# Optimization experiments

Hardware: AMD Instinct MI355X
Metric: run time of the kernel (lower is better)

The kernel has to match this reference:

```python
import jax, jax.numpy as jnp
import numpy as np

C_S, C_Z, C_H, H, PQ, PV = 384, 128, 16, 12, 4, 8
B, N = 1, 512
W_C = (2.0 / (9.0 * PQ)) ** 0.5
W_L = (1.0 / 3.0) ** 0.5
OUT_IN = H * C_Z + H * C_H + H * PV * 3 + H * PV  # 2112


def setup_inputs() -> dict:
    key = jax.random.key(0)
    ks = jax.random.split(key, 16)
    s_i = jax.random.normal(ks[0], (B, N, C_S), jnp.float32)
    z_ij = jax.random.normal(ks[1], (B, N, N, C_Z), jnp.float32)
    # random rotation matrices via QR
    raw = jax.random.normal(ks[2], (B, N, 3, 3), jnp.float32)
    q, r = jnp.linalg.qr(raw)
    rots = q * jnp.sign(jnp.diagonal(r, axis1=-2, axis2=-1))[..., None, :]
    trans = jax.random.normal(ks[3], (B, N, 3), jnp.float32)
    sc = lambda fan_in: 1.0 / np.sqrt(fan_in)
    Wq = jax.random.normal(ks[4], (C_S, H * C_H), jnp.float32) * sc(C_S)
    Wk = jax.random.normal(ks[5], (C_S, H * C_H), jnp.float32) * sc(C_S)
    Wv = jax.random.normal(ks[6], (C_S, H * C_H), jnp.float32) * sc(C_S)
    Wqp = jax.random.normal(ks[7], (C_S, H * PQ * 3), jnp.float32) * sc(C_S)
    Wkp = jax.random.normal(ks[8], (C_S, H * PQ * 3), jnp.float32) * sc(C_S)
    Wvp = jax.random.normal(ks[9], (C_S, H * PV * 3), jnp.float32) * sc(C_S)
    Wb = jax.random.normal(ks[10], (C_Z, H), jnp.float32) * sc(C_Z)
    gamma = jax.random.normal(ks[11], (1, 1, 1, H), jnp.float32)
    Wout = jax.random.normal(ks[12], (OUT_IN, C_S), jnp.float32) * sc(OUT_IN)
    bout = jnp.zeros((C_S,), jnp.float32)
    return dict(s_i=s_i, z_ij=z_ij, rots=rots, trans=trans, Wq=Wq, Wk=Wk, Wv=Wv,
                Wqp=Wqp, Wkp=Wkp, Wvp=Wvp, Wb=Wb, gamma=gamma, Wout=Wout, bout=bout)


def reference(s_i, z_ij, rots, trans, Wq, Wk, Wv, Wqp, Wkp, Wvp, Wb, gamma, Wout, bout):
    b, n = s_i.shape[0], s_i.shape[1]
    q_h = (s_i @ Wq).reshape(b, n, H, C_H)
    k_h = (s_i @ Wk).reshape(b, n, H, C_H)
    v_h = (s_i @ Wv).reshape(b, n, H, C_H)
    q_hp = (s_i @ Wqp).reshape(b, n, H, PQ, 3)
    k_hp = (s_i @ Wkp).reshape(b, n, H, PQ, 3)
    v_hp = (s_i @ Wvp).reshape(b, n, H, PV, 3)
    b_ij = z_ij @ Wb  # (b,i,j,h)

    t = trans[:, :, None, None, :]  # (b,i,1,1,3)
    apply = lambda x: jnp.einsum('bixy,bihpy->bihpx', rots, x) + t
    inv_apply = lambda x: jnp.einsum('bixy,bihpx->bihpy', rots, x - t)

    qg = apply(q_hp)  # (b,i,h,p,3) global frame
    kg = apply(k_hp)
    # pairwise rigid point distance term: (b,i,j,h)
    diff = qg[:, :, None] - kg[:, None]  # (b,i,j,h,p,3)
    dist2 = jnp.sum(diff * diff, axis=(-1, -2))

    a_s = jnp.einsum('bihd,bjhd->bijh', q_h, k_h) / (C_H ** 0.5)
    a_rigid = (W_C / 2.0) * gamma * dist2
    a = jax.nn.softmax(W_L * (a_s + b_ij - a_rigid), axis=-2)  # softmax over j

    o_hat = jnp.einsum('bijh,bijd->bihd', a, z_ij)
    o = jnp.einsum('bijh,bjhd->bihd', a, v_h)
    vg = apply(v_hp)  # (b,j,h,p,3)
    o_hp = inv_apply(jnp.einsum('bijh,bjhpx->bihpx', a, vg))  # (b,i,h,pv,3)
    o_hp_norm = jnp.sqrt(jnp.sum(o_hp * o_hp, axis=-1))  # (b,i,h,pv)

    cat = jnp.concatenate([
        o_hat.reshape(b, n, H * C_Z),
        o.reshape(b, n, H * C_H),
        o_hp.reshape(b, n, H * PV * 3),
        o_hp_norm.reshape(b, n, H * PV),
    ], axis=-1)
    return cat @ Wout + bout
```

## Files before the change

### kernel.cpp

```cpp
#include <hip/hip_runtime.h>
#include <hip/hip_bf16.h>
#include <math.h>

#define NRES 512
#define CS   384
#define CZ   128
#define NH   12
#define PW   1152
#define JB   64
#define NCH  8
#define PSTRIDE32 1040
#define KS   6
#define KAW  352

static constexpr float WL_F      = 0.57735026918962576f;
static constexpr float HALF_WC_F = 0.11785113019775792f;

typedef __attribute__((ext_vector_type(8))) short short8v;
typedef __attribute__((ext_vector_type(4))) float floatx4;

__device__ __forceinline__ ushort f2b(float f) {
    union { float f; uint u; } v; v.f = f;
    return (ushort)((v.u + 0x7FFFu + ((v.u >> 16) & 1u)) >> 16);
}
__device__ __forceinline__ float b2f(ushort b) {
    union { uint u; float f; } v; v.u = ((uint)b) << 16; return v.f;
}

__global__ __launch_bounds__(256) void k_aux(
    const float* __restrict__ P, const float* __restrict__ Wb,
    const float* __restrict__ Wout,
    ushort* __restrict__ Kfull, ushort* __restrict__ vp2,
    ushort* __restrict__ wbt16, ushort* __restrict__ woT)
{
    __shared__ ushort tile[64][72];
    __shared__ float njs[NH];
    const int bx = blockIdx.x;
    const int tid = threadIdx.x;
    if (bx < 512) {
        const int j = bx;
        const float* prow = P + (size_t)j * PW;
        const float* kr  = prow + 192;
        const float* vr  = prow + 384;
        const float* kgr = prow + 720;
        const float* vgr = prow + 864;
        if (tid < NH) {
            float s = 0.f;
            #pragma unroll
            for (int e = 0; e < 12; ++e) { const float v = kgr[tid * 12 + e]; s += v * v; }
            njs[tid] = s;
        }
        __syncthreads();
        ushort* dst = Kfull + (size_t)j * KAW;
        for (int t = tid; t < KAW; t += 256) {
            float v;
            if (t < 192)       v = kr[t];
            else if (t < 336)  v = kgr[t - 192];
            else if (t < 348)  v = njs[t - 336];
            else if (t == 348) v = 1.0f;
            else               v = 0.f;
            dst[t] = f2b(v);
        }
        const int p = j >> 1, par = j & 1;
        for (int c = tid; c < 480; c += 256) {
            const float v = (c < 192) ? vr[c] : vgr[c - 192];
            vp2[((size_t)p * 480 + c) * 2 + par] = f2b(v);
        }
    } else if (bx < 710) {
        const int t = bx - 512;
        const int k0 = (t % 33) * 64, c0 = (t / 33) * 64;
        for (int idx = tid; idx < 4096; idx += 256) {
            const int r = idx >> 6, c = idx & 63;
            tile[r][c] = f2b(Wout[(size_t)(k0 + r) * 384 + c0 + c]);
        }
        __syncthreads();
        for (int idx = tid; idx < 4096; idx += 256) {
            const int c = idx >> 6, r = idx & 63;
            woT[(size_t)(c0 + c) * 2112 + k0 + r] = tile[r][c];
        }
    } else {
        for (int idx = tid; idx < 16 * 128; idx += 256) {
            const int h = idx >> 7, cc = idx & 127;
            wbt16[idx] = (h < NH) ? f2b(WL_F * Wb[(size_t)cc * NH + h]) : (ushort)0;
        }
    }
}

__global__ __launch_bounds__(256) void k_gemm(
    const float* __restrict__ s,
    const float* __restrict__ Wq, const float* __restrict__ Wk,
    const float* __restrict__ Wv, const float* __restrict__ Wqp,
    const float* __restrict__ Wkp, const float* __restrict__ Wvp,
    const float* __restrict__ rots, const float* __restrict__ trans,
    float* __restrict__ P)
{
    const int tid = threadIdx.x;
    const int tx = tid & 15, ty = tid >> 4;
    const int n0 = blockIdx.x * 48;
    const int m0 = blockIdx.y * 32;
    __shared__ float As[32][34];
    __shared__ float Bs[32][50];
    __shared__ float rot_lds[32][12];

    const float* Wsel; int W, base;
    if (n0 < 192)      { Wsel = Wq;  W = 192; base = 0;   }
    else if (n0 < 384) { Wsel = Wk;  W = 192; base = 192; }
    else if (n0 < 576) { Wsel = Wv;  W = 192; base = 384; }
    else if (n0 < 720) { Wsel = Wqp; W = 144; base = 576; }
    else if (n0 < 864) { Wsel = Wkp; W = 144; base = 720; }
    else               { Wsel = Wvp; W = 288; base = 864; }
    const int nb = n0 - base;

    if (n0 >= 576) {
        for (int idx = tid; idx < 32 * 12; idx += 256) {
            int r = idx / 12, q = idx % 12;
            rot_lds[r][q] = (q < 9) ? rots[(size_t)(m0 + r) * 9 + q]
                                    : trans[(size_t)(m0 + r) * 3 + q - 9];
        }
    }

    float acc[2][3];
    #pragma unroll
    for (int u = 0; u < 2; ++u)
        #pragma unroll
        for (int v = 0; v < 3; ++v) acc[u][v] = 0.f;

    for (int k0 = 0; k0 < CS; k0 += 32) {
        __syncthreads();
        #pragma unroll
        for (int l = 0; l < 4; ++l) {
            int idx = tid + l * 256;
            int kk = idx & 31, r = idx >> 5;
            As[kk][r] = s[(size_t)(m0 + r) * CS + k0 + kk];
        }
        #pragma unroll
        for (int l = 0; l < 6; ++l) {
            int idx = tid + l * 256;
            int kk = idx / 48, cc = idx % 48;
            Bs[kk][cc] = Wsel[(size_t)(k0 + kk) * W + nb + cc];
        }
        __syncthreads();
        #pragma unroll
        for (int kk = 0; kk < 32; ++kk) {
            const float2 a = *(const float2*)&As[kk][ty * 2];
            const float b0 = Bs[kk][tx * 3], b1 = Bs[kk][tx * 3 + 1], b2 = Bs[kk][tx * 3 + 2];
            acc[0][0] += a.x * b0; acc[0][1] += a.x * b1; acc[0][2] += a.x * b2;
            acc[1][0] += a.y * b0; acc[1][1] += a.y * b1; acc[1][2] += a.y * b2;
        }
    }

    #pragma unroll
    for (int u = 0; u < 2; ++u) {
        float v0 = acc[u][0], v1 = acc[u][1], v2 = acc[u][2];
        if (n0 >= 576) {
            const float* RT = rot_lds[ty * 2 + u];
            const float p0 = v0, p1 = v1, p2 = v2;
            v0 = RT[0] * p0 + RT[1] * p1 + RT[2] * p2 + RT[9];
            v1 = RT[3] * p0 + RT[4] * p1 + RT[5] * p2 + RT[10];
            v2 = RT[6] * p0 + RT[7] * p1 + RT[8] * p2 + RT[11];
        }
        float* dst = P + (size_t)(m0 + ty * 2 + u) * PW + n0 + tx * 3;
        dst[0] = v0; dst[1] = v1; dst[2] = v2;
    }
}

__global__ __launch_bounds__(256, 4) void k_flash(
    const float* __restrict__ z, const ushort* __restrict__ wbt16,
    const float* __restrict__ gamma, const float* __restrict__ P,
    const ushort* __restrict__ Kfull, const ushort* __restrict__ vp2,
    uint* __restrict__ part)
{
    const int i   = blockIdx.x;
    const int jc  = blockIdx.y;
    const int j0  = jc * JB;
    const int tid = threadIdx.x;
    const int wid = tid >> 6, lane = tid & 63;

    __shared__ __align__(16) short zbT[128 * JB];
    __shared__ __align__(16) char  uni[10240];
    __shared__ float pm[NH], ps[NH];

    short*  BfT     = (short*)uni;
    float*  ltf     = (float*)uni;
    short*  ltb     = (short*)(uni + 4352);
    float4* halfacc = (float4*)(uni + 6400);

    uint* pb32   = part + ((size_t)i * NCH + jc) * PSTRIDE32;
    ushort* pb16 = (ushort*)pb32;
    float* pbf   = (float*)pb32;

    const int jb = wid * 16 + (lane & 15);
    const int ko = (lane >> 4) * 8;

    short8v af[4];
    {
        const float* za = z + ((size_t)i * NRES + j0 + jb) * CZ + ko;
        float4 fz[8];
        #pragma unroll
        for (int m = 0; m < 4; ++m) {
            fz[2 * m]     = *(const float4*)(za + m * 32);
            fz[2 * m + 1] = *(const float4*)(za + m * 32 + 4);
        }
        #pragma unroll
        for (int m = 0; m < 4; ++m) {
            const float4 f0 = fz[2 * m], f1 = fz[2 * m + 1];
            short8v a;
            a[0] = (short)f2b(f0.x); a[1] = (short)f2b(f0.y);
            a[2] = (short)f2b(f0.z); a[3] = (short)f2b(f0.w);
            a[4] = (short)f2b(f1.x); a[5] = (short)f2b(f1.y);
            a[6] = (short)f2b(f1.z); a[7] = (short)f2b(f1.w);
            af[m] = a;
            #pragma unroll
            for (int e = 0; e < 8; ++e) {
                const int c = ko + m * 32 + e;
                zbT[c * 64 + (((jb >> 3) ^ (c & 7)) * 8) + (jb & 7)] = a[e];
            }
        }
    }
    {
        const float* prow = P + (size_t)i * PW;
        for (int t = tid; t < 12 * 352; t += 256) {
            const int h = t / 352, k = t - h * 352;
            float v = 0.f;
            if (k < 192) {
                if ((k >> 4) == h) v = 0.25f * WL_F * prow[k];
            } else if (k < 336) {
                const int e = k - 192;
                if (e / 12 == h) v = 2.f * HALF_WC_F * WL_F * gamma[h] * prow[576 + e];
            } else if (k < 348) {
                if (k - 336 == h) v = -HALF_WC_F * WL_F * gamma[h];
            } else if (k == 348) {
                float ss = 0.f;
                #pragma unroll
                for (int e = 0; e < 12; ++e) {
                    const float x = prow[576 + h * 12 + e];
                    ss += x * x;
                }
                v = -HALF_WC_F * WL_F * gamma[h] * ss;
            }
            BfT[t] = (short)f2b(v);
        }
    }
    __syncthreads();

    floatx4 lacc = {0.f, 0.f, 0.f, 0.f};
    {
        const int n  = lane & 15;
        const int nb = (n < NH) ? n : 0;
        const ushort* arow = Kfull + (size_t)(j0 + jb) * KAW + ko;
        const short*  brow = &BfT[nb * 352 + ko];
        const ushort* wrow = wbt16 + n * 128 + ko;
        short8v kf[11], wv[4];
        #pragma unroll
        for (int st = 0; st < 11; ++st) kf[st] = *(const short8v*)(arow + st * 32);
        #pragma unroll
        for (int st = 0; st < 4; ++st)  wv[st] = *(const short8v*)(wrow + st * 32);
        #pragma unroll
        for (int st = 0; st < 11; ++st) {
            const short8v b = *(const short8v*)(brow + st * 32);
            lacc = __builtin_amdgcn_mfma_f32_16x16x32_bf16(kf[st], b, lacc, 0, 0, 0);
        }
        #pragma unroll
        for (int st = 0; st < 4; ++st)
            lacc = __builtin_amdgcn_mfma_f32_16x16x32_bf16(af[st], wv[st], lacc, 0, 0, 0);
    }
    __syncthreads();
    {
        const int n = lane & 15;
        #pragma unroll
        for (int r = 0; r < 4; ++r)
            ltf[n * 68 + wid * 16 + (lane >> 4) * 4 + r] = lacc[r];
    }
    __syncthreads();

    if (tid < 192) {
        const int h = tid >> 4, s = tid & 15;
        float4 v = *(const float4*)&ltf[h * 68 + s * 4];
        float m = fmaxf(fmaxf(v.x, v.y), fmaxf(v.z, v.w));
        #pragma unroll
        for (int o = 1; o < 16; o <<= 1) m = fmaxf(m, __shfl_xor(m, o));
        float4 e;
        e.x = __expf(v.x - m); e.y = __expf(v.y - m);
        e.z = __expf(v.z - m); e.w = __expf(v.w - m);
        float sum = e.x + e.y + e.z + e.w;
        #pragma unroll
        for (int o = 1; o < 16; o <<= 1) sum += __shfl_xor(sum, o);
        *(float4*)&ltf[h * 68 + s * 4] = e;
        const uint lo = (uint)f2b(e.x) | ((uint)f2b(e.y) << 16);
        const uint hi = (uint)f2b(e.z) | ((uint)f2b(e.w) << 16);
        uint* dst = (uint*)&ltb[h * 64 + (((s >> 1) ^ (h & 7)) * 8) + (s & 1) * 4];
        dst[0] = lo; dst[1] = hi;
        if (s == 0) { pm[h] = m; ps[h] = sum; }
    } else {
        const int tt = tid - 192;
        uint* dst = (uint*)&ltb[(12 + (tt >> 4)) * 64 + (tt & 15) * 4];
        dst[0] = 0u; dst[1] = 0u;
    }
    __syncthreads();

    {
        const int hrow = lane & 15;
        const int u0 = (lane >> 4), u1 = u0 + 4;
        const short8v a0 = *(const short8v*)&ltb[hrow * 64 + ((u0 ^ (hrow & 7)) * 8)];
        const short8v a1 = *(const short8v*)&ltb[hrow * 64 + ((u1 ^ (hrow & 7)) * 8)];
        #pragma unroll
        for (int t = 0; t < 2; ++t) {
            const int d = (wid * 2 + t) * 16 + (lane & 15);
            const short8v b0 = *(const short8v*)&zbT[d * 64 + ((u0 ^ (d & 7)) * 8)];
            const short8v b1 = *(const short8v*)&zbT[d * 64 + ((u1 ^ (d & 7)) * 8)];
            floatx4 acc = {0.f, 0.f, 0.f, 0.f};
            acc = __builtin_amdgcn_mfma_f32_16x16x32_bf16(a0, b0, acc, 0, 0, 0);
            acc = __builtin_amdgcn_mfma_f32_16x16x32_bf16(a1, b1, acc, 0, 0, 0);
            #pragma unroll
            for (int r = 0; r < 4; ++r) {
                const int h = u0 * 4 + r;
                if (h < NH) pb16[h * 128 + d] = f2b(acc[r]);
            }
        }
    }

    {
        if (tid < 240) {
            const int half = tid / 120, col = tid % 120;
            const int h = (col < 48) ? (col >> 2) : ((col - 48) / 6);
            const ushort* vb = vp2 + ((size_t)((j0 >> 1) + half * 16) * 480 + col * 4) * 2;
            const float* er = &ltf[h * 68 + half * 32];
            float ax = 0.f, ay = 0.f, az = 0.f, aw = 0.f;
            #pragma unroll
            for (int b = 0; b < 2; ++b) {
                uint4 raw[8];
                #pragma unroll
                for (int t = 0; t < 8; ++t)
                    raw[t] = *(const uint4*)(vb + (size_t)(b * 8 + t) * 960);
                #pragma unroll
                for (int t = 0; t < 8; ++t) {
                    const float e0 = er[2 * (b * 8 + t)], e1 = er[2 * (b * 8 + t) + 1];
                    ax += e0 * b2f((ushort)raw[t].x) + e1 * b2f((ushort)(raw[t].x >> 16));
                    ay += e0 * b2f((ushort)raw[t].y) + e1 * b2f((ushort)(raw[t].y >> 16));
                    az += e0 * b2f((ushort)raw[t].z) + e1 * b2f((ushort)(raw[t].z >> 16));
                    aw += e0 * b2f((ushort)raw[t].w) + e1 * b2f((ushort)(raw[t].w >> 16));
                }
            }
            halfacc[tid] = make_float4(ax, ay, az, aw);
        }
        __syncthreads();
        if (tid < 120) {
            const float4 s0 = halfacc[tid], s1 = halfacc[tid + 120];
            const int off16 = (tid < 48) ? 1536 + tid * 4 : 1728 + (tid - 48) * 4;
            uint* dst = (uint*)&pb16[off16];
            dst[0] = (uint)f2b(s0.x + s1.x) | ((uint)f2b(s0.y + s1.y) << 16);
            dst[1] = (uint)f2b(s0.z + s1.z) | ((uint)f2b(s0.w + s1.w) << 16);
        }
        if (tid < NH) { pbf[1008 + tid] = pm[tid]; pbf[1020 + tid] = ps[tid]; }
    }
}

__global__ __launch_bounds__(256) void k_combine(
    const uint* __restrict__ part, const float* __restrict__ rots,
    const float* __restrict__ trans, ushort* __restrict__ cat16)
{
    const int i   = blockIdx.x;
    const int tid = threadIdx.x;
    __shared__ float wgt[NCH][NH];
    __shared__ float ohp[288];

    const uint* base = part + (size_t)i * NCH * PSTRIDE32;
    if (tid < NH) {
        const int h = tid;
        float mm[NCH];
        float M = -1e30f;
        #pragma unroll
        for (int c = 0; c < NCH; ++c) {
            mm[c] = ((const float*)(base + c * PSTRIDE32))[1008 + h];
            M = fmaxf(M, mm[c]);
        }
        float S = 0.f;
        #pragma unroll
        for (int c = 0; c < NCH; ++c) {
            const float w = __expf(mm[c] - M);
            S += w * ((const float*)(base + c * PSTRIDE32))[1020 + h];
            wgt[c][h] = w;
        }
        const float inv = 1.0f / S;
        #pragma unroll
        for (int c = 0; c < NCH; ++c) wgt[c][h] *= inv;
    }
    __syncthreads();

    ushort* crow = cat16 + (size_t)i * 2112;
    uint*   crowu = (uint*)crow;
    if (tid < 192) {
        const int h = tid >> 4;
        float v[8];
        #pragma unroll
        for (int e = 0; e < 8; ++e) v[e] = 0.f;
        #pragma unroll
        for (int c = 0; c < NCH; ++c) {
            const uint4 u = *(const uint4*)&base[c * PSTRIDE32 + tid * 4];
            const float w = wgt[c][h];
            v[0] += b2f((ushort)u.x) * w; v[1] += b2f((ushort)(u.x >> 16)) * w;
            v[2] += b2f((ushort)u.y) * w; v[3] += b2f((ushort)(u.y >> 16)) * w;
            v[4] += b2f((ushort)u.z) * w; v[5] += b2f((ushort)(u.z >> 16)) * w;
            v[6] += b2f((ushort)u.w) * w; v[7] += b2f((ushort)(u.w >> 16)) * w;
        }
        uint4 o;
        o.x = (uint)f2b(v[0]) | ((uint)f2b(v[1]) << 16);
        o.y = (uint)f2b(v[2]) | ((uint)f2b(v[3]) << 16);
        o.z = (uint)f2b(v[4]) | ((uint)f2b(v[5]) << 16);
        o.w = (uint)f2b(v[6]) | ((uint)f2b(v[7]) << 16);
        *(uint4*)&crowu[tid * 4] = o;
    }
    if (tid < 96) {
        const int h = tid >> 3;
        float v0 = 0.f, v1 = 0.f;
        #pragma unroll
        for (int c = 0; c < NCH; ++c) {
            const uint u = base[c * PSTRIDE32 + 768 + tid];
            const float w = wgt[c][h];
            v0 += b2f((ushort)u) * w;
            v1 += b2f((ushort)(u >> 16)) * w;
        }
        crowu[768 + tid] = (uint)f2b(v0) | ((uint)f2b(v1) << 16);
    }
    if (tid < 144) {
        const int h = tid / 12;
        float v0 = 0.f, v1 = 0.f;
        #pragma unroll
        for (int c = 0; c < NCH; ++c) {
            const uint u = base[c * PSTRIDE32 + 864 + tid];
            const float w = wgt[c][h];
            v0 += b2f((ushort)u) * w;
            v1 += b2f((ushort)(u >> 16)) * w;
        }
        ohp[tid * 2] = v0; ohp[tid * 2 + 1] = v1;
    }
    __syncthreads();

    if (tid < 96) {
        const int h = tid >> 3, p = tid & 7;
        float R[9];
        #pragma unroll
        for (int k = 0; k < 9; ++k) R[k] = rots[(size_t)i * 9 + k];
        const float g0 = ohp[h * 24 + p * 3 + 0] - trans[(size_t)i * 3 + 0];
        const float g1 = ohp[h * 24 + p * 3 + 1] - trans[(size_t)i * 3 + 1];
        const float g2 = ohp[h * 24 + p * 3 + 2] - trans[(size_t)i * 3 + 2];
        const float oy0 = R[0] * g0 + R[3] * g1 + R[6] * g2;
        const float oy1 = R[1] * g0 + R[4] * g1 + R[7] * g2;
        const float oy2 = R[2] * g0 + R[5] * g1 + R[8] * g2;
        crow[1728 + h * 24 + p * 3 + 0] = f2b(oy0);
        crow[1728 + h * 24 + p * 3 + 1] = f2b(oy1);
        crow[1728 + h * 24 + p * 3 + 2] = f2b(oy2);
        crow[2016 + h * 8 + p] = f2b(sqrtf(oy0 * oy0 + oy1 * oy1 + oy2 * oy2));
    }
}

__global__ __launch_bounds__(256) void k_out(
    const ushort* __restrict__ cat16, const ushort* __restrict__ woT,
    float* __restrict__ opart)
{
    const int tid = threadIdx.x;
    const int wid = tid >> 6, lane = tid & 63;
    const int wm = wid >> 1, wn = wid & 1;
    const int i0 = blockIdx.x * 32 + wm * 16;
    const int c0 = blockIdx.y * 32 + wn * 16;
    const int k0 = blockIdx.z * 352;
    const ushort* arow = cat16 + (size_t)(i0 + (lane & 15)) * 2112 + k0 + (lane >> 4) * 8;
    const ushort* brow = woT   + (size_t)(c0 + (lane & 15)) * 2112 + k0 + (lane >> 4) * 8;
    floatx4 acc = {0.f, 0.f, 0.f, 0.f};
    #pragma unroll
    for (int st = 0; st < 11; ++st) {
        const short8v a = *(const short8v*)(arow + st * 32);
        const short8v b = *(const short8v*)(brow + st * 32);
        acc = __builtin_amdgcn_mfma_f32_16x16x32_bf16(a, b, acc, 0, 0, 0);
    }
    float* ob = opart + (size_t)blockIdx.z * 512 * 384;
    #pragma unroll
    for (int r = 0; r < 4; ++r) {
        const int i = i0 + (lane >> 4) * 4 + r;
        ob[(size_t)i * 384 + c0 + (lane & 15)] = acc[r];
    }
}

__global__ __launch_bounds__(256) void k_outred(
    const float* __restrict__ opart, const float* __restrict__ bout,
    float* __restrict__ out)
{
    const int e4 = blockIdx.x * 256 + threadIdx.x;
    const float4* p = (const float4*)opart;
    const float4 b = ((const float4*)bout)[e4 % 96];
    float4 r = b;
    #pragma unroll
    for (int k = 0; k < KS; ++k) {
        const float4 v = p[e4 + k * 49152];
        r.x += v.x; r.y += v.y; r.z += v.z; r.w += v.w;
    }
    ((float4*)out)[e4] = r;
}

extern "C" void kernel_launch(void* const* d_in, const int* in_sizes, int n_in,
                              void* d_out, int out_size, void* d_ws, size_t ws_size,
                              hipStream_t stream)
{
    const float* s_i   = (const float*)d_in[0];
    const float* z_ij  = (const float*)d_in[1];
    const float* rots  = (const float*)d_in[2];
    const float* trans = (const float*)d_in[3];
    const float* Wq    = (const float*)d_in[4];
    const float* Wk    = (const float*)d_in[5];
    const float* Wv    = (const float*)d_in[6];
    const float* Wqp   = (const float*)d_in[7];
    const float* Wkp   = (const float*)d_in[8];
    const float* Wvp   = (const float*)d_in[9];
    const float* Wb    = (const float*)d_in[10];
    const float* gamma = (const float*)d_in[11];
    const float* Wout  = (const float*)d_in[12];
    const float* bout  = (const float*)d_in[13];
    float* ws = (float*)d_ws;
    float*  P     = ws;
    uint*   part  = (uint*)(P + 589824);
    float*  opart = (float*)part;
    ushort* cat16 = (ushort*)(part + (size_t)512 * NCH * PSTRIDE32);
    ushort* wbt16 = cat16 + 1081344;
    ushort* kfull = wbt16 + 2048;
    ushort* woT   = kfull + 512 * KAW;
    ushort* vp2   = woT + (size_t)384 * 2112;
    float*  out   = (float*)d_out;

    hipLaunchKernelGGL(k_gemm, dim3(24, 16), dim3(256), 0, stream,
                       s_i, Wq, Wk, Wv, Wqp, Wkp, Wvp, rots, trans, P);
    hipLaunchKernelGGL(k_aux, dim3(711), dim3(256), 0, stream,
                       P, Wb, Wout, kfull, vp2, wbt16, woT);
    hipLaunchKernelGGL(k_flash, dim3(512, NCH), dim3(256), 0, stream,
                       z_ij, wbt16, gamma, P, kfull, vp2, part);
    hipLaunchKernelGGL(k_combine, dim3(512), dim3(256), 0, stream,
                       part, rots, trans, cat16);
    hipLaunchKernelGGL(k_out, dim3(16, 12, KS), dim3(256), 0, stream,
                       cat16, woT, opart);
    hipLaunchKernelGGL(k_outred, dim3(192), dim3(256), 0, stream,
                       opart, bout, out);
}
```

Before: 116.2 us.

## Loop four key chunks per flash block with online softmax rescaling

The attention kernel's grid drops from eight key chunks per query to two halves. Each block now loops over four 64-key chunks and keeps running max, sum and output accumulators, rescaling them as the max changes. This spreads the per-block query-side setup (building the bias/point B matrix and loading Wb fragments) over more keys. It also cuts the partial-result buffer and the combine kernel's reduction from eight partials to two. In exchange the grid has a quarter as many blocks, and each block runs serial chunks separated by barriers with no prefetch, which may hide memory latency less well.

```diff
diff --git a/kernel.cpp b/kernel.cpp
--- a/kernel.cpp
+++ b/kernel.cpp
@@ -8,7 +8,7 @@
 #define NH   12
 #define PW   1152
 #define JB   64
-#define NCH  8
+#define NCHP 2
 #define PSTRIDE32 1040
 #define KS   6
 #define KAW  352
@@ -170,54 +170,36 @@
     const ushort* __restrict__ Kfull, const ushort* __restrict__ vp2,
     uint* __restrict__ part)
 {
-    const int i   = blockIdx.x;
-    const int jc  = blockIdx.y;
-    const int j0  = jc * JB;
-    const int tid = threadIdx.x;
-    const int wid = tid >> 6, lane = tid & 63;
+    const int i    = blockIdx.x;
+    const int half = blockIdx.y;
+    const int tid  = threadIdx.x;
+    const int wid  = tid >> 6, lane = tid & 63;
 
     __shared__ __align__(16) short zbT[128 * JB];
-    __shared__ __align__(16) char  uni[10240];
-    __shared__ float pm[NH], ps[NH];
-
-    short*  BfT     = (short*)uni;
-    float*  ltf     = (float*)uni;
-    short*  ltb     = (short*)(uni + 4352);
-    float4* halfacc = (float4*)(uni + 6400);
-
-    uint* pb32   = part + ((size_t)i * NCH + jc) * PSTRIDE32;
+    __shared__ __align__(16) short BfT[12 * 352];
+    __shared__ __align__(16) float ltf[12 * 68];
+    __shared__ __align__(16) short ltb[16 * 64];
+    __shared__ __align__(16) float4 halfacc[240];
+    __shared__ float pm[NH], pS[NH], corr[NH];
+
+    uint* pb32   = part + ((size_t)i * NCHP + half) * PSTRIDE32;
     ushort* pb16 = (ushort*)pb32;
     float* pbf   = (float*)pb32;
 
     const int jb = wid * 16 + (lane & 15);
     const int ko = (lane >> 4) * 8;
-
-    short8v af[4];
+    const int n  = lane & 15;
+    const int nb = (n < NH) ? n : 0;
+
+    const int ecol  = (tid < 240) ? (tid % 120) : 0;
+    const int eh2   = (tid < 240) ? (tid / 120) : 0;
+    const int eh    = (ecol < 48) ? (ecol >> 2) : ((ecol - 48) / 6);
+
+    short8v wv[4];
     {
-        const float* za = z + ((size_t)i * NRES + j0 + jb) * CZ + ko;
-        float4 fz[8];
-        #pragma unroll
-        for (int m = 0; m < 4; ++m) {
-            fz[2 * m]     = *(const float4*)(za + m * 32);
-            fz[2 * m + 1] = *(const float4*)(za + m * 32 + 4);
-        }
-        #pragma unroll
-        for (int m = 0; m < 4; ++m) {
-            const float4 f0 = fz[2 * m], f1 = fz[2 * m + 1];
-            short8v a;
-            a[0] = (short)f2b(f0.x); a[1] = (short)f2b(f0.y);
-            a[2] = (short)f2b(f0.z); a[3] = (short)f2b(f0.w);
-            a[4] = (short)f2b(f1.x); a[5] = (short)f2b(f1.y);
-            a[6] = (short)f2b(f1.z); a[7] = (short)f2b(f1.w);
-            af[m] = a;
-            #pragma unroll
-            for (int e = 0; e < 8; ++e) {
-                const int c = ko + m * 32 + e;
-                zbT[c * 64 + (((jb >> 3) ^ (c & 7)) * 8) + (jb & 7)] = a[e];
-            }
-        }
-    }
-    {
+        const ushort* wrow = wbt16 + n * 128 + ko;
+        #pragma unroll
+        for (int st = 0; st < 4; ++st) wv[st] = *(const short8v*)(wrow + st * 32);
         const float* prow = P + (size_t)i * PW;
         for (int t = tid; t < 12 * 352; t += 256) {
             const int h = t / 352, k = t - h * 352;
@@ -240,92 +222,124 @@
             }
             BfT[t] = (short)f2b(v);
         }
-    }
+        if (tid < NH) { pm[tid] = -1e30f; pS[tid] = 0.f; }
+    }
+
+    floatx4 oacc[2];
+    oacc[0] = (floatx4){0.f, 0.f, 0.f, 0.f};
+    oacc[1] = (floatx4){0.f, 0.f, 0.f, 0.f};
+    float eax = 0.f, eay = 0.f, eaz = 0.f, eaw = 0.f;
+
     __syncthreads();
 
-    floatx4 lacc = {0.f, 0.f, 0.f, 0.f};
-    {
-        const int n  = lane & 15;
-        const int nb = (n < NH) ? n : 0;
-        const ushort* arow = Kfull + (size_t)(j0 + jb) * KAW + ko;
-        const short*  brow = &BfT[nb * 352 + ko];
-        const ushort* wrow = wbt16 + n * 128 + ko;
-        short8v kf[11], wv[4];
-        #pragma unroll
-        for (int st = 0; st < 11; ++st) kf[st] = *(const short8v*)(arow + st * 32);
-        #pragma unroll
-        for (int st = 0; st < 4; ++st)  wv[st] = *(const short8v*)(wrow + st * 32);
-        #pragma unroll
-        for (int st = 0; st < 11; ++st) {
-            const short8v b = *(const short8v*)(brow + st * 32);
-            lacc = __builtin_amdgcn_mfma_f32_16x16x32_bf16(kf[st], b, lacc, 0, 0, 0);
-        }
-        #pragma unroll
-        for (int st = 0; st < 4; ++st)
-            lacc = __builtin_amdgcn_mfma_f32_16x16x32_bf16(af[st], wv[st], lacc, 0, 0, 0);
-    }
-    __syncthreads();
-    {
-        const int n = lane & 15;
-        #pragma unroll
-        for (int r = 0; r < 4; ++r)
-            ltf[n * 68 + wid * 16 + (lane >> 4) * 4 + r] = lacc[r];
-    }
-    __syncthreads();
-
-    if (tid < 192) {
-        const int h = tid >> 4, s = tid & 15;
-        float4 v = *(const float4*)&ltf[h * 68 + s * 4];
-        float m = fmaxf(fmaxf(v.x, v.y), fmaxf(v.z, v.w));
-        #pragma unroll
-        for (int o = 1; o < 16; o <<= 1) m = fmaxf(m, __shfl_xor(m, o));
-        float4 e;
-        e.x = __expf(v.x - m); e.y = __expf(v.y - m);
-        e.z = __expf(v.z - m); e.w = __expf(v.w - m);
-        float sum = e.x + e.y + e.z + e.w;
-        #pragma unroll
-        for (int o = 1; o < 16; o <<= 1) sum += __shfl_xor(sum, o);
-        *(float4*)&ltf[h * 68 + s * 4] = e;
-        const uint lo = (uint)f2b(e.x) | ((uint)f2b(e.y) << 16);
-        const uint hi = (uint)f2b(e.z) | ((uint)f2b(e.w) << 16);
-        uint* dst = (uint*)&ltb[h * 64 + (((s >> 1) ^ (h & 7)) * 8) + (s & 1) * 4];
-        dst[0] = lo; dst[1] = hi;
-        if (s == 0) { pm[h] = m; ps[h] = sum; }
-    } else {
-        const int tt = tid - 192;
-        uint* dst = (uint*)&ltb[(12 + (tt >> 4)) * 64 + (tt & 15) * 4];
-        dst[0] = 0u; dst[1] = 0u;
-    }
-    __syncthreads();
-
-    {
-        const int hrow = lane & 15;
-        const int u0 = (lane >> 4), u1 = u0 + 4;
-        const short8v a0 = *(const short8v*)&ltb[hrow * 64 + ((u0 ^ (hrow & 7)) * 8)];
-        const short8v a1 = *(const short8v*)&ltb[hrow * 64 + ((u1 ^ (hrow & 7)) * 8)];
-        #pragma unroll
-        for (int t = 0; t < 2; ++t) {
-            const int d = (wid * 2 + t) * 16 + (lane & 15);
-            const short8v b0 = *(const short8v*)&zbT[d * 64 + ((u0 ^ (d & 7)) * 8)];
-            const short8v b1 = *(const short8v*)&zbT[d * 64 + ((u1 ^ (d & 7)) * 8)];
-            floatx4 acc = {0.f, 0.f, 0.f, 0.f};
-            acc = __builtin_amdgcn_mfma_f32_16x16x32_bf16(a0, b0, acc, 0, 0, 0);
-            acc = __builtin_amdgcn_mfma_f32_16x16x32_bf16(a1, b1, acc, 0, 0, 0);
-            #pragma unroll
-            for (int r = 0; r < 4; ++r) {
-                const int h = u0 * 4 + r;
-                if (h < NH) pb16[h * 128 + d] = f2b(acc[r]);
-            }
-        }
-    }
-
-    {
+    for (int c = 0; c < 4; ++c) {
+        const int j0 = (half * 4 + c) * JB;
+
+        short8v af[4], kf[11];
+        {
+            const float* za = z + ((size_t)i * NRES + j0 + jb) * CZ + ko;
+            float4 fz[8];
+            #pragma unroll
+            for (int m = 0; m < 4; ++m) {
+                fz[2 * m]     = *(const float4*)(za + m * 32);
+                fz[2 * m + 1] = *(const float4*)(za + m * 32 + 4);
+            }
+            const ushort* arow = Kfull + (size_t)(j0 + jb) * KAW + ko;
+            #pragma unroll
+            for (int st = 0; st < 11; ++st) kf[st] = *(const short8v*)(arow + st * 32);
+            #pragma unroll
+            for (int m = 0; m < 4; ++m) {
+                const float4 f0 = fz[2 * m], f1 = fz[2 * m + 1];
+                short8v a;
+                a[0] = (short)f2b(f0.x); a[1] = (short)f2b(f0.y);
+                a[2] = (short)f2b(f0.z); a[3] = (short)f2b(f0.w);
+                a[4] = (short)f2b(f1.x); a[5] = (short)f2b(f1.y);
+                a[6] = (short)f2b(f1.z); a[7] = (short)f2b(f1.w);
+                af[m] = a;
+                #pragma unroll
+                for (int e = 0; e < 8; ++e) {
+                    const int cc = ko + m * 32 + e;
+                    zbT[cc * 64 + (((jb >> 3) ^ (cc & 7)) * 8) + (jb & 7)] = a[e];
+                }
+            }
+        }
+
+        {
+            floatx4 lacc = {0.f, 0.f, 0.f, 0.f};
+            const short* brow = &BfT[nb * 352 + ko];
+            #pragma unroll
+            for (int st = 0; st < 11; ++st) {
+                const short8v b = *(const short8v*)(brow + st * 32);
+                lacc = __builtin_amdgcn_mfma_f32_16x16x32_bf16(kf[st], b, lacc, 0, 0, 0);
+            }
+            #pragma unroll
+            for (int st = 0; st < 4; ++st)
+                lacc = __builtin_amdgcn_mfma_f32_16x16x32_bf16(af[st], wv[st], lacc, 0, 0, 0);
+            if (n < NH) {
+                #pragma unroll
+                for (int r = 0; r < 4; ++r)
+                    ltf[n * 68 + wid * 16 + (lane >> 4) * 4 + r] = lacc[r];
+            }
+        }
+        __syncthreads();
+
+        if (tid < 192) {
+            const int h = tid >> 4, s = tid & 15;
+            float4 v = *(const float4*)&ltf[h * 68 + s * 4];
+            float mc = fmaxf(fmaxf(v.x, v.y), fmaxf(v.z, v.w));
+            #pragma unroll
+            for (int o = 1; o < 16; o <<= 1) mc = fmaxf(mc, __shfl_xor(mc, o));
+            const float mold = pm[h];
+            const float mnew = fmaxf(mold, mc);
+            float4 e;
+            e.x = __expf(v.x - mnew); e.y = __expf(v.y - mnew);
+            e.z = __expf(v.z - mnew); e.w = __expf(v.w - mnew);
+            float sum = e.x + e.y + e.z + e.w;
+            #pragma unroll
+            for (int o = 1; o < 16; o <<= 1) sum += __shfl_xor(sum, o);
+            *(float4*)&ltf[h * 68 + s * 4] = e;
+            const uint lo = (uint)f2b(e.x) | ((uint)f2b(e.y) << 16);
+            const uint hi = (uint)f2b(e.z) | ((uint)f2b(e.w) << 16);
+            uint* dst = (uint*)&ltb[h * 64 + (((s >> 1) ^ (h & 7)) * 8) + (s & 1) * 4];
+            dst[0] = lo; dst[1] = hi;
+            if (s == 0) {
+                const float cf = __expf(mold - mnew);
+                corr[h] = cf;
+                pS[h] = pS[h] * cf + sum;
+                pm[h] = mnew;
+            }
+        } else {
+            const int tt = tid - 192;
+            uint* dst = (uint*)&ltb[(12 + (tt >> 4)) * 64 + (tt & 15) * 4];
+            dst[0] = 0u; dst[1] = 0u;
+        }
+        __syncthreads();
+
+        {
+            const int hrow = lane & 15;
+            const int u0 = (lane >> 4), u1 = u0 + 4;
+            const short8v a0 = *(const short8v*)&ltb[hrow * 64 + ((u0 ^ (hrow & 7)) * 8)];
+            const short8v a1 = *(const short8v*)&ltb[hrow * 64 + ((u1 ^ (hrow & 7)) * 8)];
+            #pragma unroll
+            for (int t = 0; t < 2; ++t) {
+                #pragma unroll
+                for (int r = 0; r < 4; ++r) {
+                    const int h = u0 * 4 + r;
+                    if (h < NH) oacc[t][r] *= corr[h];
+                }
+                const int d = (wid * 2 + t) * 16 + (lane & 15);
+                const short8v b0 = *(const short8v*)&zbT[d * 64 + ((u0 ^ (d & 7)) * 8)];
+                const short8v b1 = *(const short8v*)&zbT[d * 64 + ((u1 ^ (d & 7)) * 8)];
+                oacc[t] = __builtin_amdgcn_mfma_f32_16x16x32_bf16(a0, b0, oacc[t], 0, 0, 0);
+                oacc[t] = __builtin_amdgcn_mfma_f32_16x16x32_bf16(a1, b1, oacc[t], 0, 0, 0);
+            }
+        }
+
         if (tid < 240) {
-            const int half = tid / 120, col = tid % 120;
-            const int h = (col < 48) ? (col >> 2) : ((col - 48) / 6);
-            const ushort* vb = vp2 + ((size_t)((j0 >> 1) + half * 16) * 480 + col * 4) * 2;
-            const float* er = &ltf[h * 68 + half * 32];
-            float ax = 0.f, ay = 0.f, az = 0.f, aw = 0.f;
+            const float cf = corr[eh];
+            eax *= cf; eay *= cf; eaz *= cf; eaw *= cf;
+            const ushort* vb = vp2 + ((size_t)((j0 >> 1) + eh2 * 16) * 480 + ecol * 4) * 2;
+            const float* er = &ltf[eh * 68 + eh2 * 32];
             #pragma unroll
             for (int b = 0; b < 2; ++b) {
                 uint4 raw[8];
@@ -335,24 +349,38 @@
                 #pragma unroll
                 for (int t = 0; t < 8; ++t) {
                     const float e0 = er[2 * (b * 8 + t)], e1 = er[2 * (b * 8 + t) + 1];
-                    ax += e0 * b2f((ushort)raw[t].x) + e1 * b2f((ushort)(raw[t].x >> 16));
-                    ay += e0 * b2f((ushort)raw[t].y) + e1 * b2f((ushort)(raw[t].y >> 16));
-                    az += e0 * b2f((ushort)raw[t].z) + e1 * b2f((ushort)(raw[t].z >> 16));
-                    aw += e0 * b2f((ushort)raw[t].w) + e1 * b2f((ushort)(raw[t].w >> 16));
+                    eax += e0 * b2f((ushort)raw[t].x) + e1 * b2f((ushort)(raw[t].x >> 16));
+                    eay += e0 * b2f((ushort)raw[t].y) + e1 * b2f((ushort)(raw[t].y >> 16));
+                    eaz += e0 * b2f((ushort)raw[t].z) + e1 * b2f((ushort)(raw[t].z >> 16));
+                    eaw += e0 * b2f((ushort)raw[t].w) + e1 * b2f((ushort)(raw[t].w >> 16));
                 }
             }
-            halfacc[tid] = make_float4(ax, ay, az, aw);
-        }
-        __syncthreads();
-        if (tid < 120) {
-            const float4 s0 = halfacc[tid], s1 = halfacc[tid + 120];
-            const int off16 = (tid < 48) ? 1536 + tid * 4 : 1728 + (tid - 48) * 4;
-            uint* dst = (uint*)&pb16[off16];
-            dst[0] = (uint)f2b(s0.x + s1.x) | ((uint)f2b(s0.y + s1.y) << 16);
-            dst[1] = (uint)f2b(s0.z + s1.z) | ((uint)f2b(s0.w + s1.w) << 16);
-        }
-        if (tid < NH) { pbf[1008 + tid] = pm[tid]; pbf[1020 + tid] = ps[tid]; }
-    }
+        }
+        __syncthreads();
+    }
+
+    {
+        const int u0 = (lane >> 4);
+        #pragma unroll
+        for (int t = 0; t < 2; ++t) {
+            const int d = (wid * 2 + t) * 16 + (lane & 15);
+            #pragma unroll
+            for (int r = 0; r < 4; ++r) {
+                const int h = u0 * 4 + r;
+                if (h < NH) pb16[h * 128 + d] = f2b(oacc[t][r]);
+            }
+        }
+        if (tid < 240) halfacc[tid] = make_float4(eax, eay, eaz, eaw);
+    }
+    __syncthreads();
+    if (tid < 120) {
+        const float4 s0 = halfacc[tid], s1 = halfacc[tid + 120];
+        const int off16 = (tid < 48) ? 1536 + tid * 4 : 1728 + (tid - 48) * 4;
+        uint* dst = (uint*)&pb16[off16];
+        dst[0] = (uint)f2b(s0.x + s1.x) | ((uint)f2b(s0.y + s1.y) << 16);
+        dst[1] = (uint)f2b(s0.z + s1.z) | ((uint)f2b(s0.w + s1.w) << 16);
+    }
+    if (tid < NH) { pbf[1008 + tid] = pm[tid]; pbf[1020 + tid] = pS[tid]; }
 }
 
 __global__ __launch_bounds__(256) void k_combine(
@@ -361,29 +389,29 @@
 {
     const int i   = blockIdx.x;
     const int tid = threadIdx.x;
-    __shared__ float wgt[NCH][NH];
+    __shared__ float wgt[NCHP][NH];
     __shared__ float ohp[288];
 
-    const uint* base = part + (size_t)i * NCH * PSTRIDE32;
+    const uint* base = part + (size_t)i * NCHP * PSTRIDE32;
     if (tid < NH) {
         const int h = tid;
-        float mm[NCH];
+        float mm[NCHP];
         float M = -1e30f;
         #pragma unroll
-        for (int c = 0; c < NCH; ++c) {
+        for (int c = 0; c < NCHP; ++c) {
             mm[c] = ((const float*)(base + c * PSTRIDE32))[1008 + h];
             M = fmaxf(M, mm[c]);
         }
         float S = 0.f;
         #pragma unroll
-        for (int c = 0; c < NCH; ++c) {
+        for (int c = 0; c < NCHP; ++c) {
             const float w = __expf(mm[c] - M);
             S += w * ((const float*)(base + c * PSTRIDE32))[1020 + h];
             wgt[c][h] = w;
         }
         const float inv = 1.0f / S;
         #pragma unroll
-        for (int c = 0; c < NCH; ++c) wgt[c][h] *= inv;
+        for (int c = 0; c < NCHP; ++c) wgt[c][h] *= inv;
     }
     __syncthreads();
 
@@ -395,7 +423,7 @@
         #pragma unroll
         for (int e = 0; e < 8; ++e) v[e] = 0.f;
         #pragma unroll
-        for (int c = 0; c < NCH; ++c) {
+        for (int c = 0; c < NCHP; ++c) {
             const uint4 u = *(const uint4*)&base[c * PSTRIDE32 + tid * 4];
             const float w = wgt[c][h];
             v[0] += b2f((ushort)u.x) * w; v[1] += b2f((ushort)(u.x >> 16)) * w;
@@ -414,7 +442,7 @@
         const int h = tid >> 3;
         float v0 = 0.f, v1 = 0.f;
         #pragma unroll
-        for (int c = 0; c < NCH; ++c) {
+        for (int c = 0; c < NCHP; ++c) {
             const uint u = base[c * PSTRIDE32 + 768 + tid];
             const float w = wgt[c][h];
             v0 += b2f((ushort)u) * w;
@@ -426,7 +454,7 @@
         const int h = tid / 12;
         float v0 = 0.f, v1 = 0.f;
         #pragma unroll
-        for (int c = 0; c < NCH; ++c) {
+        for (int c = 0; c < NCHP; ++c) {
             const uint u = base[c * PSTRIDE32 + 864 + tid];
             const float w = wgt[c][h];
             v0 += b2f((ushort)u) * w;
@@ -519,7 +547,7 @@
     float*  P     = ws;
     uint*   part  = (uint*)(P + 589824);
     float*  opart = (float*)part;
-    ushort* cat16 = (ushort*)(part + (size_t)512 * NCH * PSTRIDE32);
+    ushort* cat16 = (ushort*)(part + 1179648);
     ushort* wbt16 = cat16 + 1081344;
     ushort* kfull = wbt16 + 2048;
     ushort* woT   = kfull + 512 * KAW;
@@ -530,7 +558,7 @@
                        s_i, Wq, Wk, Wv, Wqp, Wkp, Wvp, rots, trans, P);
     hipLaunchKernelGGL(k_aux, dim3(711), dim3(256), 0, stream,
                        P, Wb, Wout, kfull, vp2, wbt16, woT);
-    hipLaunchKernelGGL(k_flash, dim3(512, NCH), dim3(256), 0, stream,
+    hipLaunchKernelGGL(k_flash, dim3(512, NCHP), dim3(256), 0, stream,
                        z_ij, wbt16, gamma, P, kfull, vp2, part);
     hipLaunchKernelGGL(k_combine, dim3(512), dim3(256), 0, stream,
                        part, rots, trans, cat16);
```

After: 117.1 us. No clear change (+0.8%).
